# Kernel tuning notes

Hardware: AMD Instinct MI355X
Metric: run time of the kernel (lower is better)

The kernel has to match this reference:

```python
import jax, jax.numpy as jnp
import numpy as np

B, T, D, N = 2, 2048, 1024, 16
H = D // N  # 64

def setup_inputs() -> dict:
    key = jax.random.key(0)
    ks = jax.random.split(key, 5)
    s = 0.02
    return {
        "x": jax.random.normal(ks[0], (B, T, D), dtype=jnp.float32),
        "w_attn": jax.random.normal(ks[1], (D, 3 * D), dtype=jnp.float32) * s,
        "b_attn": jax.random.normal(ks[2], (3 * D,), dtype=jnp.float32) * s,
        "w_proj": jax.random.normal(ks[3], (D, D), dtype=jnp.float32) * s,
        "b_proj": jax.random.normal(ks[4], (D,), dtype=jnp.float32) * s,
    }

def reference(x, w_attn, b_attn, w_proj, b_proj):
    # qkv projection: (B,T,3D)
    qkv = jnp.einsum('btd,de->bte', x, w_attn) + b_attn
    q, k, v = jnp.split(qkv, 3, axis=-1)
    q = q.reshape(B, T, N, H)
    k = k.reshape(B, T, N, H)
    v = v.reshape(B, T, N, H)
    scale = jnp.asarray(H ** 0.5, dtype=x.dtype)
    # scores: (B, T_q, T_kv, N) -- matches torch einsum 'btnh,bsnh->btsn'
    scores = jnp.einsum('btnh,bsnh->btsn', q, k) / scale
    # causal mask, past_len = 0 (no kv cache)
    causal = jnp.tril(jnp.ones((T, T), dtype=bool))  # (T_q, T_kv)
    scores = jnp.where(causal[None, :, :, None], scores, jnp.asarray(-jnp.inf, dtype=scores.dtype))
    weights = jax.nn.softmax(scores, axis=2)  # softmax over kv axis
    out = jnp.einsum('btsn,bsnh->btnh', weights, v).reshape(B, T, D)
    output = jnp.einsum('btd,de->bte', out, w_proj) + b_proj
    return output, k, v
```

## Files before the change

kernel.cpp:

```cpp
#include <hip/hip_runtime.h>
#include <hip/hip_bf16.h>


typedef __attribute__((ext_vector_type(8))) short bf16x8;
typedef __attribute__((ext_vector_type(4))) float f32x4;

#define MFMA16(a, b, c) __builtin_amdgcn_mfma_f32_16x16x32_bf16(a, b, c, 0, 0, 0)

static constexpr int Bb = 2, Tt = 2048, Dd = 1024, Nn = 16, Hh = 64;
static constexpr float NEG_BIG = -30000.0f;
static constexpr float QSCALE  = 0.125f;

__device__ __forceinline__ short f2bf(float f) {
    __hip_bfloat16 h = __float2bfloat16(f);
    short s; __builtin_memcpy(&s, &h, 2); return s;
}
__device__ __forceinline__ float bf2f(short s) {
    __hip_bfloat16 h; __builtin_memcpy(&h, &s, 2); return __bfloat162float(h);
}
__device__ __forceinline__ bf16x8 cvt8(const float* __restrict__ p) {
    f32x4 a = *(const f32x4*)p, b = *(const f32x4*)(p + 4);
    bf16x8 r;
    #pragma unroll
    for (int j = 0; j < 4; ++j) { r[j] = f2bf(a[j]); r[4 + j] = f2bf(b[j]); }
    return r;
}
__device__ __forceinline__ bf16x8 cvt8s(const float* __restrict__ p, float s) {
    f32x4 a = *(const f32x4*)p, b = *(const f32x4*)(p + 4);
    bf16x8 r;
    #pragma unroll
    for (int j = 0; j < 4; ++j) { r[j] = f2bf(a[j] * s); r[4 + j] = f2bf(b[j] * s); }
    return r;
}

__device__ __forceinline__ void gload16(const short* g, short* l) {
    __builtin_amdgcn_global_load_lds(
        (const __attribute__((address_space(1))) unsigned int*)g,
        (__attribute__((address_space(3))) unsigned int*)l, 16, 0, 0);
}

template<int CTRL>
__device__ __forceinline__ float dppf(float x) {
    int i; __builtin_memcpy(&i, &x, 4);
    i = __builtin_amdgcn_update_dpp(0, i, CTRL, 0xf, 0xf, true);
    float r; __builtin_memcpy(&r, &i, 4); return r;
}
__device__ __forceinline__ float rowmax16(float x) {
    x = fmaxf(x, dppf<0x128>(x)); x = fmaxf(x, dppf<0x124>(x));
    x = fmaxf(x, dppf<0x122>(x)); x = fmaxf(x, dppf<0x121>(x));
    return x;
}
__device__ __forceinline__ float rowsum16(float x) {
    x += dppf<0x128>(x); x += dppf<0x124>(x);
    x += dppf<0x122>(x); x += dppf<0x121>(x);
    return x;
}

__global__ __launch_bounds__(256) void prep(
    const float* __restrict__ x, const float* __restrict__ wa,
    const float* __restrict__ wp,
    short* __restrict__ xb, short* __restrict__ wat, short* __restrict__ wpt)
{
    const int bid = blockIdx.x, tid = threadIdx.x;
    if (bid < 1024) {
        __shared__ float s[64][65];
        const float* src; short* dst; int Nc, k0, n0;
        if (bid < 768) { src = wa; dst = wat; Nc = 3072; k0 = (bid & 15) * 64; n0 = (bid >> 4) * 64; }
        else { int b2 = bid - 768; src = wp; dst = wpt; Nc = 1024; k0 = (b2 & 15) * 64; n0 = (b2 >> 4) * 64; }
        const int row = tid >> 2, cg = (tid & 3) * 16;
        const float* p = src + (size_t)(k0 + row) * Nc + n0 + cg;
        #pragma unroll
        for (int i = 0; i < 4; ++i) {
            f32x4 v = *(const f32x4*)(p + 4 * i);
            #pragma unroll
            for (int j = 0; j < 4; ++j) s[row][cg + 4 * i + j] = v[j];
        }
        __syncthreads();
        bf16x8 o0, o1;
        #pragma unroll
        for (int j = 0; j < 8; ++j) { o0[j] = f2bf(s[cg + j][row]); o1[j] = f2bf(s[cg + 8 + j][row]); }
        short* q = dst + (size_t)(n0 + row) * 1024 + k0 + cg;
        *(bf16x8*)q = o0; *(bf16x8*)(q + 8) = o1;
    } else {
        const size_t base = (size_t)(bid - 1024) * 2048 + tid * 8;
        *(bf16x8*)(xb + base) = cvt8(x + base);
    }
}

template<int MODE>
__global__ __launch_bounds__(256) void gemm128(
    const short* __restrict__ A, const short* __restrict__ Bt,
    const float* __restrict__ bias,
    float* __restrict__ fk, float* __restrict__ fv,
    short* __restrict__ qb, short* __restrict__ kb, short* __restrict__ vt,
    float* __restrict__ fout, int K)
{
    __shared__ short sA[3][128][32];
    __shared__ short sB[3][128][32];
    const int tid = threadIdx.x, lane = tid & 63, wave = tid >> 6;
    const int l15 = lane & 15, quad = lane >> 4;

    const int lid = (int)blockIdx.y * (int)gridDim.x + (int)blockIdx.x;
    const int xcd = lid & 7, sidx = lid >> 3;
    constexpr int SN = (MODE == 1) ? 12 : 4;
    const int mt = (xcd & 3) * 8 + (sidx & 7);
    const int ntl = (xcd >> 2) * SN + (sidx >> 3);
    const int m0 = mt * 128, n0 = ntl * 128;

    const int wr = (wave >> 1) * 64, wc = (wave & 1) * 64;

    const int rl  = lane >> 2;
    const int csh = (lane & 3) * 8;
    const size_t aOff0 = (size_t)(m0 + wave * 16 + rl) * K + csh;
    const size_t aOff1 = aOff0 + (size_t)64 * K;
    const size_t bOff0 = (size_t)(n0 + wave * 16 + rl) * K + csh;
    const size_t bOff1 = bOff0 + (size_t)64 * K;

    f32x4 acc[4][4] = {};

#define STAGE_G(pp, kk)                                            \
    do {                                                           \
        gload16(A  + aOff0 + (kk), &sA[pp][wave * 16][0]);         \
        gload16(A  + aOff1 + (kk), &sA[pp][64 + wave * 16][0]);    \
        gload16(Bt + bOff0 + (kk), &sB[pp][wave * 16][0]);         \
        gload16(Bt + bOff1 + (kk), &sB[pp][64 + wave * 16][0]);    \
    } while (0)

    STAGE_G(0, 0);
    STAGE_G(1, 32);

    int cur = 0;
    for (int k0 = 0; k0 < K; k0 += 32) {
        if (k0 + 32 < K) {
            asm volatile("s_waitcnt vmcnt(4)" ::: "memory");
        } else {
            asm volatile("s_waitcnt vmcnt(0)" ::: "memory");
        }
        __builtin_amdgcn_s_barrier();
        __builtin_amdgcn_sched_barrier(0);

        const int nxt2 = cur >= 1 ? cur - 1 : cur + 2;
        if (k0 + 64 < K) STAGE_G(nxt2, k0 + 64);

        bf16x8 af[4], bfr[4];
        #pragma unroll
        for (int mt2 = 0; mt2 < 4; ++mt2) af[mt2]  = *(const bf16x8*)&sA[cur][wr + mt2 * 16 + l15][quad * 8];
        #pragma unroll
        for (int nt2 = 0; nt2 < 4; ++nt2) bfr[nt2] = *(const bf16x8*)&sB[cur][wc + nt2 * 16 + l15][quad * 8];
        #pragma unroll
        for (int mt2 = 0; mt2 < 4; ++mt2)
        #pragma unroll
        for (int nt2 = 0; nt2 < 4; ++nt2)
            acc[mt2][nt2] = MFMA16(af[mt2], bfr[nt2], acc[mt2][nt2]);

        cur = cur < 2 ? cur + 1 : 0;
    }
#undef STAGE_G

    #pragma unroll
    for (int mt2 = 0; mt2 < 4; ++mt2)
    #pragma unroll
    for (int nt2 = 0; nt2 < 4; ++nt2) {
        const int gc = n0 + wc + nt2 * 16 + l15;
        const float bv = bias[gc];
        #pragma unroll
        for (int r = 0; r < 4; ++r) {
            const int grow = m0 + wr + mt2 * 16 + quad * 4 + r;
            const float val = acc[mt2][nt2][r] + bv;
            if (MODE == 1) {
                const int reg = gc >> 10, c = gc & 1023;
                if (reg == 0) {
                    qb[(size_t)grow * 1024 + c] = f2bf(val * QSCALE);
                } else {
                    const int bidx = grow >> 11, tt = grow & 2047;
                    const int nh = c >> 6, h = c & 63;
                    if (reg == 1) {
                        fk[(size_t)grow * 1024 + c] = val;
                        kb[((size_t)(bidx * Nn + nh) * Tt + tt) * Hh + h] = f2bf(val);
                    } else {
                        fv[(size_t)grow * 1024 + c] = val;
                        vt[((size_t)(bidx * Nn + nh) * Hh + h) * Tt + tt] = f2bf(val);
                    }
                }
            } else {
                fout[(size_t)grow * 1024 + gc] = val;
            }
        }
    }
}

__global__ __launch_bounds__(512, 6) void attn5(
    const short* __restrict__ Qb, const short* __restrict__ Kb,
    const short* __restrict__ Vt,
    short* __restrict__ op_part, float* __restrict__ ls_part)
{
    const int by = 15 - (int)blockIdx.y;
    const int c  = blockIdx.z;
    if (c && by < 8) return;

    __shared__ short sK[2][64][64];
    __shared__ short sV[2][64][64];
    __shared__ short sP[8][16][72];

    const int tid = threadIdx.x, lane = tid & 63, wave = tid >> 6;
    const int l15 = lane & 15, quad = lane >> 4;
    const int head = blockIdx.x;
    const int b = head >> 4, n = head & 15;
    const int q0w = by * 128 + wave * 16;

    const int gmask = (q0w + 15) >> 6;
    const int g0 = c * 16;
    const int ntmax = min(16, 2 * by + 2 - g0);

    const size_t kvhead = (size_t)head * Tt * Hh;
    const short* kbh = Kb + kvhead;
    const short* vth = Vt + kvhead;

    const short* qp = Qb + ((size_t)b * Tt + q0w + l15) * Dd + n * Hh + quad * 8;
    const bf16x8 qf0 = *(const bf16x8*)qp;
    const bf16x8 qf1 = *(const bf16x8*)(qp + 32);

    const int sr   = wave * 8 + (lane >> 3);
    const int srcb = (((lane & 7) ^ (lane >> 3))) * 8;
    const int swz  = l15 & 7;
    const int bsw  = quad ^ swz;

    f32x4 o_acc[4] = {};
    float lsum[4] = {};

#define STAGE_KV(bb, ktb)                                               \
    do {                                                                \
        gload16(kbh + (size_t)((ktb) + sr) * Hh + srcb, &sK[bb][wave * 8][0]); \
        gload16(vth + (size_t)sr * Tt + (ktb) + srcb,   &sV[bb][wave * 8][0]); \
    } while (0)

    STAGE_KV(0, g0 * 64);
    __syncthreads();

    int buf = 0;
    for (int it = 0; it < ntmax; ++it) {
        const int kt = (g0 + it) * 64;
        if (it + 1 < ntmax) STAGE_KV(buf ^ 1, kt + 64);

        f32x4 s[4] = {};
        #pragma unroll
        for (int jp = 0; jp < 2; ++jp) {
            bf16x8 ka0 = *(const bf16x8*)&sK[buf][32 * jp      + l15][bsw * 8];
            bf16x8 kc0 = *(const bf16x8*)&sK[buf][32 * jp      + l15][(bsw ^ 4) * 8];
            bf16x8 ka1 = *(const bf16x8*)&sK[buf][32 * jp + 16 + l15][bsw * 8];
            bf16x8 kc1 = *(const bf16x8*)&sK[buf][32 * jp + 16 + l15][(bsw ^ 4) * 8];
            __builtin_amdgcn_s_setprio(1);
            s[2 * jp]     = MFMA16(qf0, ka0, s[2 * jp]);
            s[2 * jp]     = MFMA16(qf1, kc0, s[2 * jp]);
            s[2 * jp + 1] = MFMA16(qf0, ka1, s[2 * jp + 1]);
            s[2 * jp + 1] = MFMA16(qf1, kc1, s[2 * jp + 1]);
            __builtin_amdgcn_s_setprio(0);
        }

        const bool masked = (g0 + it >= gmask);
        #pragma unroll
        for (int r = 0; r < 4; ++r) {
            const int row = q0w + quad * 4 + r;
            float x0 = s[0][r], x1 = s[1][r], x2 = s[2][r], x3 = s[3][r];
            if (masked) {
                if (kt + l15      > row) x0 = NEG_BIG;
                if (kt + 16 + l15 > row) x1 = NEG_BIG;
                if (kt + 32 + l15 > row) x2 = NEG_BIG;
                if (kt + 48 + l15 > row) x3 = NEG_BIG;
            }
            const float p0 = __expf(x0), p1 = __expf(x1);
            const float p2 = __expf(x2), p3 = __expf(x3);
            lsum[r] += (p0 + p1) + (p2 + p3);
            short* pw = &sP[wave][quad * 4 + r][l15];
            pw[0] = f2bf(p0); pw[16] = f2bf(p1); pw[32] = f2bf(p2); pw[48] = f2bf(p3);
        }
        __asm__ volatile("s_waitcnt lgkmcnt(0)" ::: "memory");
        bf16x8 pf0 = *(const bf16x8*)&sP[wave][l15][quad * 8];
        bf16x8 pf1 = *(const bf16x8*)&sP[wave][l15][32 + quad * 8];
        #pragma unroll
        for (int hc = 0; hc < 4; ++hc) {
            bf16x8 v0 = *(const bf16x8*)&sV[buf][hc * 16 + l15][bsw * 8];
            bf16x8 v1 = *(const bf16x8*)&sV[buf][hc * 16 + l15][(bsw ^ 4) * 8];
            __builtin_amdgcn_s_setprio(1);
            o_acc[hc] = MFMA16(pf0, v0, o_acc[hc]);
            o_acc[hc] = MFMA16(pf1, v1, o_acc[hc]);
            __builtin_amdgcn_s_setprio(0);
        }
        __syncthreads();
        buf ^= 1;
    }
#undef STAGE_KV

    const int slot = head * 24 + (by < 8 ? by : 2 * by - 8 + c);
    short* opw = op_part + ((size_t)slot * 128 + wave * 16) * 64;
    #pragma unroll
    for (int r = 0; r < 4; ++r) {
        const float l = rowsum16(lsum[r]);
        const int rloc = quad * 4 + r;
        if (l15 == 0) ls_part[slot * 128 + wave * 16 + rloc] = l;
        #pragma unroll
        for (int hc = 0; hc < 4; ++hc)
            opw[rloc * 64 + hc * 16 + l15] = f2bf(o_acc[hc][r]);
    }
}

__global__ __launch_bounds__(256) void attn_reduce(
    const short* __restrict__ op_part, const float* __restrict__ ls_part,
    short* __restrict__ Ob)
{
    const int idx = blockIdx.x * 256 + threadIdx.x;
    const int r = idx >> 3;
    const int h0 = (idx & 7) * 8;
    const int head = r >> 11, t = r & 2047;
    const int by = t >> 7, tr = t & 127;
    const int nch = 1 + (by >= 8);
    const int base = head * 24 + (by < 8 ? by : 2 * by - 8);

    float acc[8] = {};
    float l = 0.f;
    for (int c = 0; c < nch; ++c) {
        const int slot = base + c;
        bf16x8 v = *(const bf16x8*)(op_part + ((size_t)slot * 128 + tr) * 64 + h0);
        #pragma unroll
        for (int j = 0; j < 8; ++j) acc[j] += bf2f(v[j]);
        l += ls_part[slot * 128 + tr];
    }
    const float rl = 1.0f / fmaxf(l, 1e-20f);
    bf16x8 o;
    #pragma unroll
    for (int j = 0; j < 8; ++j) o[j] = f2bf(acc[j] * rl);
    const int b = head >> 4, n = head & 15;
    *(bf16x8*)(Ob + ((size_t)(b * Tt + t)) * Dd + n * Hh + h0) = o;
}

__global__ __launch_bounds__(256) void gemm_bias_split(
    const float* __restrict__ A, const float* __restrict__ Bm,
    const float* __restrict__ bias,
    float* __restrict__ dst0, float* __restrict__ dst1, float* __restrict__ dst2,
    short* __restrict__ kb, short* __restrict__ vt,
    int K, int Ncols, int Dsplit)
{
    __shared__ short sA[64][40];
    __shared__ short sBt[64][40];
    const int tid  = threadIdx.x;
    const int lane = tid & 63;
    const int wave = tid >> 6;
    const int l15  = lane & 15;
    const int quad = lane >> 4;
    const int m0 = blockIdx.x * 64;
    const int n0 = blockIdx.y * 64;
    const int wm = (wave >> 1) * 32;
    const int wn = (wave & 1) * 32;
    const int ar = tid >> 2, ac = (tid & 3) * 8;
    const int bk = tid >> 3, bc = (tid & 7) * 8;

    f32x4 acc[2][2] = {};
    for (int k0 = 0; k0 < K; k0 += 32) {
        bf16x8 av = cvt8(A  + (size_t)(m0 + ar) * K     + k0 + ac);
        bf16x8 bv = cvt8(Bm + (size_t)(k0 + bk) * Ncols + n0 + bc);
        *(bf16x8*)&sA[ar][ac] = av;
        #pragma unroll
        for (int j = 0; j < 8; ++j) sBt[bc + j][bk] = bv[j];
        __syncthreads();
        bf16x8 a0 = *(const bf16x8*)&sA[wm + l15][quad * 8];
        bf16x8 a1 = *(const bf16x8*)&sA[wm + 16 + l15][quad * 8];
        bf16x8 b0 = *(const bf16x8*)&sBt[wn + l15][quad * 8];
        bf16x8 b1 = *(const bf16x8*)&sBt[wn + 16 + l15][quad * 8];
        acc[0][0] = MFMA16(a0, b0, acc[0][0]);
        acc[0][1] = MFMA16(a0, b1, acc[0][1]);
        acc[1][0] = MFMA16(a1, b0, acc[1][0]);
        acc[1][1] = MFMA16(a1, b1, acc[1][1]);
        __syncthreads();
    }
    #pragma unroll
    for (int i = 0; i < 2; ++i)
    #pragma unroll
    for (int j = 0; j < 2; ++j) {
        const int ncol = n0 + wn + j * 16 + l15;
        const float bvf = bias[ncol];
        float* dbase; int c, which;
        if (ncol < Dsplit)        { dbase = dst0; c = ncol;            which = 0; }
        else if (ncol < 2*Dsplit) { dbase = dst1; c = ncol - Dsplit;   which = 1; }
        else                      { dbase = dst2; c = ncol - 2*Dsplit; which = 2; }
        const int nh = c >> 6, h = c & 63;
        #pragma unroll
        for (int r = 0; r < 4; ++r) {
            const int mrow = m0 + wm + i * 16 + quad * 4 + r;
            const float val = acc[i][j][r] + bvf;
            dbase[(size_t)mrow * Dsplit + c] = val;
            if (which == 1 && kb) {
                const int bidx = mrow >> 11, tt = mrow & 2047;
                kb[((size_t)(bidx * Nn + nh) * Tt + tt) * Hh + h] = f2bf(val);
            } else if (which == 2 && vt) {
                const int bidx = mrow >> 11, tt = mrow & 2047;
                vt[((size_t)(bidx * Nn + nh) * Hh + h) * Tt + tt] = f2bf(val);
            }
        }
    }
}

__global__ __launch_bounds__(256) void attn_fast(
    const float* __restrict__ Q, const short* __restrict__ Kb,
    const short* __restrict__ Vt, float* __restrict__ O)
{
    __shared__ short sP[4][2][16][40];
    const int tid  = threadIdx.x;
    const int lane = tid & 63;
    const int wave = tid >> 6;
    const int l15  = lane & 15;
    const int quad = lane >> 4;
    const int b = blockIdx.x >> 4, n = blockIdx.x & 15;
    const int qg = ((int)gridDim.y - 1 - (int)blockIdx.y) * 4 + wave;
    const int q0 = qg * 16;

    const size_t ohead  = (size_t)b * Tt * Dd + (size_t)n * Hh;
    const size_t kvhead = (size_t)(b * Nn + n) * Tt * Hh;
    const short* kbh = Kb + kvhead;
    const short* vth = Vt + kvhead;

    const float* qrow = Q + ohead + (size_t)(q0 + l15) * Dd;
    const bf16x8 qf0 = cvt8s(qrow + quad * 8, QSCALE);
    const bf16x8 qf1 = cvt8s(qrow + 32 + quad * 8, QSCALE);

    float m_i[4], l_i[4];
    f32x4 o_acc[4] = {};
    #pragma unroll
    for (int r = 0; r < 4; ++r) { m_i[r] = NEG_BIG; l_i[r] = 0.f; }

    int par = 0;
    for (int kt = 0; kt < q0 + 16; kt += 32, par ^= 1) {
        f32x4 s0 = {}, s1 = {};
        {
            const short* k0 = kbh + (size_t)(kt + l15) * Hh + quad * 8;
            bf16x8 k0a = *(const bf16x8*)k0;
            bf16x8 k0b = *(const bf16x8*)(k0 + 32);
            const short* k1 = k0 + 16 * Hh;
            bf16x8 k1a = *(const bf16x8*)k1;
            bf16x8 k1b = *(const bf16x8*)(k1 + 32);
            s0 = MFMA16(qf0, k0a, s0); s0 = MFMA16(qf1, k0b, s0);
            s1 = MFMA16(qf0, k1a, s1); s1 = MFMA16(qf1, k1b, s1);
        }
        const int qr0 = q0 + quad * 4;
        #pragma unroll
        for (int r = 0; r < 4; ++r) {
            float x0 = (kt + l15      > qr0 + r) ? NEG_BIG : s0[r];
            float x1 = (kt + 16 + l15 > qr0 + r) ? NEG_BIG : s1[r];
            const float t  = rowmax16(fmaxf(x0, x1));
            const float mn = fmaxf(m_i[r], t);
            const float alpha = __expf(m_i[r] - mn);
            const float p0 = __expf(x0 - mn);
            const float p1 = __expf(x1 - mn);
            l_i[r] = l_i[r] * alpha + rowsum16(p0 + p1);
            m_i[r] = mn;
            #pragma unroll
            for (int hc = 0; hc < 4; ++hc) o_acc[hc][r] *= alpha;
            sP[wave][par][quad * 4 + r][l15]      = f2bf(p0);
            sP[wave][par][quad * 4 + r][16 + l15] = f2bf(p1);
        }
        __asm__ volatile("s_waitcnt lgkmcnt(0)" ::: "memory");
        bf16x8 pf = *(const bf16x8*)&sP[wave][par][l15][quad * 8];
        #pragma unroll
        for (int hc = 0; hc < 4; ++hc) {
            bf16x8 vf = *(const bf16x8*)(vth + (size_t)(hc * 16 + l15) * Tt + kt + quad * 8);
            o_acc[hc] = MFMA16(pf, vf, o_acc[hc]);
        }
    }
    #pragma unroll
    for (int r = 0; r < 4; ++r) {
        const float rl = 1.0f / fmaxf(l_i[r], 1e-20f);
        #pragma unroll
        for (int hc = 0; hc < 4; ++hc)
            O[ohead + (size_t)(q0 + quad * 4 + r) * Dd + hc * 16 + l15] = o_acc[hc][r] * rl;
    }
}

extern "C" void kernel_launch(void* const* d_in, const int* in_sizes, int n_in,
                              void* d_out, int out_size, void* d_ws, size_t ws_size,
                              hipStream_t stream) {
    const float* x      = (const float*)d_in[0];
    const float* w_attn = (const float*)d_in[1];
    const float* b_attn = (const float*)d_in[2];
    const float* w_proj = (const float*)d_in[3];
    const float* b_proj = (const float*)d_in[4];

    const size_t elems = (size_t)Bb * Tt * Dd;
    float* out  = (float*)d_out;
    float* kout = out  + elems;
    float* vout = kout + elems;

    const size_t NSLOT = (size_t)32 * 24;
    const size_t need_v2 = (4 * elems + (size_t)1024 * 1024 + NSLOT * 128 * 64) * 2
                         + NSLOT * 128 * 4;

    if (ws_size >= need_v2) {
        short* qb  = (short*)d_ws;
        short* kb  = qb + elems;
        short* vt  = kb + elems;
        short* wpt = vt + elems;
        short* xb  = wpt + (size_t)1024 * 1024;
        short* ob  = xb;
        short* op_part = xb + elems;
        float* ls_part = (float*)(op_part + NSLOT * 128 * 64);
        short* wat = op_part;

        prep<<<3072, 256, 0, stream>>>(x, w_attn, w_proj, xb, wat, wpt);
        gemm128<1><<<dim3(32, 24), 256, 0, stream>>>(
            xb, wat, b_attn, kout, vout, qb, kb, vt, nullptr, Dd);
        attn5<<<dim3(Bb * Nn, 16, 2), 512, 0, stream>>>(qb, kb, vt, op_part, ls_part);
        attn_reduce<<<2048, 256, 0, stream>>>(op_part, ls_part, ob);
        gemm128<2><<<dim3(32, 8), 256, 0, stream>>>(
            ob, wpt, b_proj, nullptr, nullptr, nullptr, nullptr, nullptr, out, Dd);
    } else {
        float* o_ws = (float*)d_ws;
        short* kb = (short*)((char*)d_ws + elems * 4);
        short* vt = kb + elems;
        gemm_bias_split<<<dim3((Bb * Tt) / 64, (3 * Dd) / 64), 256, 0, stream>>>(
            x, w_attn, b_attn, out, kout, vout, kb, vt, Dd, 3 * Dd, Dd);
        attn_fast<<<dim3(Bb * Nn, Tt / 64), 256, 0, stream>>>(out, kb, vt, o_ws);
        gemm_bias_split<<<dim3((Bb * Tt) / 64, Dd / 64), 256, 0, stream>>>(
            o_ws, w_proj, b_proj, out, out, out, nullptr, nullptr, Dd, Dd, Dd);
    }
}
```

Baseline: 202.2 us.

## Load GEMM fragments directly from global memory into registers, dropping LDS staging

Removes the shared-memory triple-buffered staging in the 128x128 GEMM. Each wave now loads its A/B MFMA fragments straight from global memory into registers, double-buffered across k-steps, and launch bounds request 3 blocks per CU. This removes the LDS traffic and barriers. In exchange, operand reuse across waves is lost: each A/B row is fetched by two waves, which doubles global/L2 traffic, and the 16-byte loads per lane are strided by K.

```diff
diff --git a/kernel.cpp b/kernel.cpp
--- a/kernel.cpp
+++ b/kernel.cpp
@@ -88,15 +88,13 @@
 }
 
 template<int MODE>
-__global__ __launch_bounds__(256) void gemm128(
+__global__ __launch_bounds__(256, 3) void gemm128(
     const short* __restrict__ A, const short* __restrict__ Bt,
     const float* __restrict__ bias,
     float* __restrict__ fk, float* __restrict__ fv,
     short* __restrict__ qb, short* __restrict__ kb, short* __restrict__ vt,
     float* __restrict__ fout, int K)
 {
-    __shared__ short sA[3][128][32];
-    __shared__ short sB[3][128][32];
     const int tid = threadIdx.x, lane = tid & 63, wave = tid >> 6;
     const int l15 = lane & 15, quad = lane >> 4;
 
@@ -109,53 +107,44 @@
 
     const int wr = (wave >> 1) * 64, wc = (wave & 1) * 64;
 
-    const int rl  = lane >> 2;
-    const int csh = (lane & 3) * 8;
-    const size_t aOff0 = (size_t)(m0 + wave * 16 + rl) * K + csh;
-    const size_t aOff1 = aOff0 + (size_t)64 * K;
-    const size_t bOff0 = (size_t)(n0 + wave * 16 + rl) * K + csh;
-    const size_t bOff1 = bOff0 + (size_t)64 * K;
+    const short* pa = A  + (size_t)(m0 + wr + l15) * K + quad * 8;
+    const short* pb = Bt + (size_t)(n0 + wc + l15) * K + quad * 8;
+    const size_t rstep = (size_t)16 * K;
 
     f32x4 acc[4][4] = {};
-
-#define STAGE_G(pp, kk)                                            \
-    do {                                                           \
-        gload16(A  + aOff0 + (kk), &sA[pp][wave * 16][0]);         \
-        gload16(A  + aOff1 + (kk), &sA[pp][64 + wave * 16][0]);    \
-        gload16(Bt + bOff0 + (kk), &sB[pp][wave * 16][0]);         \
-        gload16(Bt + bOff1 + (kk), &sB[pp][64 + wave * 16][0]);    \
-    } while (0)
-
-    STAGE_G(0, 0);
-    STAGE_G(1, 32);
-
-    int cur = 0;
-    for (int k0 = 0; k0 < K; k0 += 32) {
-        if (k0 + 32 < K) {
-            asm volatile("s_waitcnt vmcnt(4)" ::: "memory");
-        } else {
-            asm volatile("s_waitcnt vmcnt(0)" ::: "memory");
-        }
-        __builtin_amdgcn_s_barrier();
-        __builtin_amdgcn_sched_barrier(0);
-
-        const int nxt2 = cur >= 1 ? cur - 1 : cur + 2;
-        if (k0 + 64 < K) STAGE_G(nxt2, k0 + 64);
-
-        bf16x8 af[4], bfr[4];
-        #pragma unroll
-        for (int mt2 = 0; mt2 < 4; ++mt2) af[mt2]  = *(const bf16x8*)&sA[cur][wr + mt2 * 16 + l15][quad * 8];
-        #pragma unroll
-        for (int nt2 = 0; nt2 < 4; ++nt2) bfr[nt2] = *(const bf16x8*)&sB[cur][wc + nt2 * 16 + l15][quad * 8];
-        #pragma unroll
-        for (int mt2 = 0; mt2 < 4; ++mt2)
-        #pragma unroll
-        for (int nt2 = 0; nt2 < 4; ++nt2)
-            acc[mt2][nt2] = MFMA16(af[mt2], bfr[nt2], acc[mt2][nt2]);
-
-        cur = cur < 2 ? cur + 1 : 0;
-    }
-#undef STAGE_G
+    bf16x8 a0[4], b0[4], a1[4], b1[4];
+
+    #pragma unroll
+    for (int i = 0; i < 4; ++i) {
+        a0[i] = *(const bf16x8*)(pa + (size_t)i * rstep);
+        b0[i] = *(const bf16x8*)(pb + (size_t)i * rstep);
+    }
+
+    for (int k0 = 0; k0 < K; k0 += 64) {
+        #pragma unroll
+        for (int i = 0; i < 4; ++i) {
+            a1[i] = *(const bf16x8*)(pa + (size_t)i * rstep + k0 + 32);
+            b1[i] = *(const bf16x8*)(pb + (size_t)i * rstep + k0 + 32);
+        }
+        #pragma unroll
+        for (int i = 0; i < 4; ++i)
+        #pragma unroll
+        for (int j = 0; j < 4; ++j)
+            acc[i][j] = MFMA16(a0[i], b0[j], acc[i][j]);
+
+        if (k0 + 64 < K) {
+            #pragma unroll
+            for (int i = 0; i < 4; ++i) {
+                a0[i] = *(const bf16x8*)(pa + (size_t)i * rstep + k0 + 64);
+                b0[i] = *(const bf16x8*)(pb + (size_t)i * rstep + k0 + 64);
+            }
+        }
+        #pragma unroll
+        for (int i = 0; i < 4; ++i)
+        #pragma unroll
+        for (int j = 0; j < 4; ++j)
+            acc[i][j] = MFMA16(a1[i], b1[j], acc[i][j]);
+    }
 
     #pragma unroll
     for (int mt2 = 0; mt2 < 4; ++mt2)
```

Measured after the change: 274.6 us. 35.8% more time.
